# Kernel tuning notes

Measured on AMD Instinct MI355X. Metric: run time of the kernel, lower is better.

The kernel has to match this reference:

```python
import jax, jax.numpy as jnp
import numpy as np

B, S, D, H = 1, 3072, 2048, 16
HD = D // H          # head_dim = 128
C = HD // 2          # rotary complex pairs = 64
EPS = 1e-6
WINDOW = 3           # frames of sliding-window attention on each side
L_TOKENS = 256       # tokens per frame (forward arg L)
NUM_FRAMES = S // L_TOKENS


def setup_inputs() -> dict:
    key = jax.random.key(0)
    ks = jax.random.split(key, 5)
    scale = 1.0 / np.sqrt(D)
    x = jax.random.normal(ks[0], (B, S, D), jnp.float32)
    wq = jax.random.normal(ks[1], (D, D), jnp.float32) * scale
    wk = jax.random.normal(ks[2], (D, D), jnp.float32) * scale
    wv = jax.random.normal(ks[3], (D, D), jnp.float32) * scale
    wo = jax.random.normal(ks[4], (D, D), jnp.float32) * scale
    bq = jnp.zeros((D,), jnp.float32)
    bk = jnp.zeros((D,), jnp.float32)
    bv = jnp.zeros((D,), jnp.float32)
    bo = jnp.zeros((D,), jnp.float32)
    gq = jnp.ones((D,), jnp.float32)
    gk = jnp.ones((D,), jnp.float32)
    # rotary freqs as cos/sin of angle t * theta_c (source uses a complex [S,1,C] tensor)
    t = jnp.arange(S, dtype=jnp.float32)
    inv_freq = 1.0 / (10000.0 ** (jnp.arange(C, dtype=jnp.float32) / C))
    ang = t[:, None] * inv_freq[None, :]        # [S, C]
    cos = jnp.cos(ang)[:, None, :]              # [S, 1, C]
    sin = jnp.sin(ang)[:, None, :]              # [S, 1, C]
    return {"x": x, "wq": wq, "bq": bq, "wk": wk, "bk": bk, "wv": wv,
            "bv": bv, "wo": wo, "bo": bo, "gq": gq, "gk": gk,
            "cos": cos, "sin": sin, "f": NUM_FRAMES, "L": L_TOKENS}


def _rms_norm(h, g, eps=EPS):
    # tensor_parallel_rms_norm with tp_size=1: fp32 variance, rsqrt, scale by weight
    hf = h.astype(jnp.float32)
    var = jnp.mean(hf * hf, axis=-1, keepdims=True)
    return (hf * jax.lax.rsqrt(var + eps) * g).astype(h.dtype)


def _rope(h, cos, sin):
    # complex rotation on interleaved (real, imag) pairs per head (rope_apply_for3d)
    b, s, d = h.shape
    hd = 2 * cos.shape[-1]
    n = d // hd
    hr = h.reshape(b, s, n, hd)
    xr, xi = hr[..., 0::2], hr[..., 1::2]       # [b,s,n,C]
    c, sn = cos[None], sin[None]                # [1,s,1,C] broadcast over heads
    yr = xr * c - xi * sn
    yi = xr * sn + xi * c
    y = jnp.stack([yr, yi], axis=-1).reshape(b, s, n, hd)
    return y.reshape(b, s, d)


def reference(x, wq, bq, wk, bk, wv, bv, wo, bo, gq, gk, cos, sin, f, L):
    q = _rope(_rms_norm(x @ wq.T + bq, gq), cos, sin)
    k = _rope(_rms_norm(x @ wk.T + bk, gk), cos, sin)
    v = x @ wv.T + bv
    b, s, d = q.shape
    hd = 2 * cos.shape[-1]
    n = d // hd
    qh = q.reshape(b, s, n, hd)
    kh = k.reshape(b, s, n, hd)
    vh = v.reshape(b, s, n, hd)
    scale = 1.0 / np.sqrt(hd)
    scores = jnp.einsum('bqnd,bknd->bnqk', qh, kh) * scale
    win = L * WINDOW
    idx = jnp.arange(s)
    delta = idx[None, :] - idx[:, None]
    mask = (delta <= win) & (delta >= -win)
    scores = jnp.where(mask[None, None], scores, -jnp.inf)
    probs = jax.nn.softmax(scores, axis=-1)
    out = jnp.einsum('bnqk,bknd->bqnd', probs, vh).reshape(b, s, d)
    return out @ wo.T + bo
```

## Files before the change

### kernel.cpp

```cpp
#include <hip/hip_runtime.h>
#include <stdint.h>

typedef unsigned short u16;
typedef __attribute__((ext_vector_type(8))) short short8;
typedef __attribute__((ext_vector_type(4))) float f32x4;

#define S_LEN 3072
#define D_DIM 2048
#define WIN 768
#define INV_SQRT_HD 0.08838834764831845f
#define M_SHIFT 12.0f

__device__ __forceinline__ u16 f2bf(float x) {
  union { float f; uint32_t u; } v; v.f = x;
  uint32_t r = v.u + 0x7FFFu + ((v.u >> 16) & 1u);
  return (u16)(r >> 16);
}
__device__ __forceinline__ float bf2f(u16 x) {
  union { uint32_t u; float f; } v; v.u = ((uint32_t)x) << 16;
  return v.f;
}

__device__ __forceinline__ void load_lds16(const void* g, void* l) {
  __builtin_amdgcn_global_load_lds(
      (const __attribute__((address_space(1))) void*)g,
      (__attribute__((address_space(3))) void*)l, 16, 0, 0);
}

#define MFMA16(a, b, c) __builtin_amdgcn_mfma_f32_16x16x32_bf16((a), (b), (c), 0, 0, 0)

__global__ __launch_bounds__(256) void k_cvt_all(const float* __restrict__ x,
                                                 const float* __restrict__ w0, const float* __restrict__ w1,
                                                 const float* __restrict__ w2, const float* __restrict__ w3,
                                                 const float* __restrict__ bq, const float* __restrict__ bk,
                                                 const float* __restrict__ bv,
                                                 u16* __restrict__ xo,
                                                 u16* __restrict__ o0, u16* __restrict__ o1,
                                                 u16* __restrict__ o2, u16* __restrict__ o3,
                                                 float* __restrict__ bias_all,
                                                 int n4x, int n4w) {
  int i = blockIdx.x * 256 + threadIdx.x;
  if (i < n4x + 4 * n4w) {
    const float* in;
    u16* out;
    int off;
    if (i < n4x) {
      in = x; out = xo; off = i;
    } else {
      int j = i - n4x;
      int seg = j / n4w;
      off = j - seg * n4w;
      in = seg == 0 ? w0 : seg == 1 ? w1 : seg == 2 ? w2 : w3;
      out = seg == 0 ? o0 : seg == 1 ? o1 : seg == 2 ? o2 : o3;
    }
    float4 v = ((const float4*)in)[off];
    ushort4 o;
    o.x = f2bf(v.x); o.y = f2bf(v.y); o.z = f2bf(v.z); o.w = f2bf(v.w);
    ((ushort4*)out)[off] = o;
  } else {
    int j = i - n4x - 4 * n4w;
    int seg = j >> 9, off = j & 511;
    const float* in = seg == 0 ? bq : seg == 1 ? bk : bv;
    ((float4*)bias_all)[j] = ((const float4*)in)[off];
  }
}

__global__ __launch_bounds__(256, 3) void k_gemm_qkv(const u16* __restrict__ A,
                                                     const u16* __restrict__ Ball,
                                                     const float* __restrict__ bias_all,
                                                     u16* __restrict__ QKV) {
  __shared__ u16 lA[128 * 32];
  __shared__ u16 lB[192 * 32];
  const int id = blockIdx.x;
  const int xcd = id & 7, local = id >> 3;
  const int m_idx = xcd * 3 + local / 32;
  const int n_idx = local % 32;
  const int m0 = m_idx * 128;
  const int n0g = n_idx * 192;
  const int t = threadIdx.x;
  const int lane = t & 63, w = t >> 6, lo = lane & 15, g = lane >> 4;
  const int wr = w >> 1, wc = w & 1;

  const int srow = t >> 2;
  const int sch = (t & 3) ^ ((srow ^ (srow >> 3)) & 3);
  const u16* ga = A + (size_t)(m0 + srow) * D_DIM + sch * 8;
  const u16* gb = Ball + (size_t)(n0g + srow) * D_DIM + sch * 8;

  const f32x4 zero4 = {0.f, 0.f, 0.f, 0.f};
  f32x4 acc[4][6];
#pragma unroll
  for (int m = 0; m < 4; ++m)
#pragma unroll
    for (int n = 0; n < 6; ++n) acc[m][n] = zero4;

  for (int k0 = 0; k0 < D_DIM; k0 += 32) {
    load_lds16(ga + k0, &lA[t * 8]);
    load_lds16(ga + (size_t)64 * D_DIM + k0, &lA[2048 + t * 8]);
    load_lds16(gb + k0, &lB[t * 8]);
    load_lds16(gb + (size_t)64 * D_DIM + k0, &lB[2048 + t * 8]);
    load_lds16(gb + (size_t)128 * D_DIM + k0, &lB[4096 + t * 8]);
    __syncthreads();
    short8 af[4], bfr[6];
#pragma unroll
    for (int m = 0; m < 4; ++m) {
      const int R = wr * 64 + m * 16 + lo;
      af[m] = *(const short8*)&lA[R * 32 + ((g ^ ((R ^ (R >> 3)) & 3)) << 3)];
    }
#pragma unroll
    for (int n = 0; n < 6; ++n) {
      const int R = wc * 96 + n * 16 + lo;
      bfr[n] = *(const short8*)&lB[R * 32 + ((g ^ ((R ^ (R >> 3)) & 3)) << 3)];
    }
#pragma unroll
    for (int m = 0; m < 4; ++m)
#pragma unroll
      for (int n = 0; n < 6; ++n) acc[m][n] = MFMA16(af[m], bfr[n], acc[m][n]);
    __syncthreads();
  }

#pragma unroll
  for (int m = 0; m < 4; ++m) {
    const int row = m0 + wr * 64 + m * 16 + 4 * g;
#pragma unroll
    for (int n = 0; n < 6; ++n) {
      const int col_g = n0g + wc * 96 + n * 16 + lo;
      const int seg_c = col_g >> 11, c = col_g & 2047;
      u16* D = QKV + (size_t)seg_c * S_LEN * D_DIM;
      const float bb = bias_all[col_g];
#pragma unroll
      for (int r = 0; r < 4; ++r)
        D[(size_t)(row + r) * D_DIM + c] = f2bf(acc[m][n][r] + bb);
    }
  }
}

__device__ __forceinline__ void gemm_body(const u16* __restrict__ A, const u16* __restrict__ B,
                                          int m0, int n0, int t, f32x4 (*acc)[4],
                                          u16* lA, u16* lB) {
  const int lane = t & 63, w = t >> 6, lo = lane & 15, g = lane >> 4;
  const int wr = w >> 1, wc = w & 1;
  const int srow = t >> 2;
  const int sch = (t & 3) ^ ((srow ^ (srow >> 3)) & 3);
  const u16* ga = A + (size_t)(m0 + srow) * D_DIM + sch * 8;
  const u16* gb = B + (size_t)(n0 + srow) * D_DIM + sch * 8;
  for (int k0 = 0; k0 < D_DIM; k0 += 32) {
    load_lds16(ga + k0, &lA[t * 8]);
    load_lds16(ga + (size_t)64 * D_DIM + k0, &lA[2048 + t * 8]);
    load_lds16(gb + k0, &lB[t * 8]);
    load_lds16(gb + (size_t)64 * D_DIM + k0, &lB[2048 + t * 8]);
    __syncthreads();
    short8 af[4], bfr[4];
#pragma unroll
    for (int m = 0; m < 4; ++m) {
      const int R = wr * 64 + m * 16 + lo;
      af[m] = *(const short8*)&lA[R * 32 + ((g ^ ((R ^ (R >> 3)) & 3)) << 3)];
    }
#pragma unroll
    for (int n = 0; n < 4; ++n) {
      const int R = wc * 64 + n * 16 + lo;
      bfr[n] = *(const short8*)&lB[R * 32 + ((g ^ ((R ^ (R >> 3)) & 3)) << 3)];
    }
#pragma unroll
    for (int m = 0; m < 4; ++m)
#pragma unroll
      for (int n = 0; n < 4; ++n) acc[m][n] = MFMA16(af[m], bfr[n], acc[m][n]);
    __syncthreads();
  }
}

__global__ __launch_bounds__(256) void k_gemm_wo(const u16* __restrict__ A,
                                                 const u16* __restrict__ B,
                                                 const float* __restrict__ bias,
                                                 float* __restrict__ C) {
  __shared__ u16 lA[128 * 32];
  __shared__ u16 lB[128 * 32];
  const int id = blockIdx.x;
  const int xcd = id & 7, local = id >> 3;
  const int m_idx = xcd * 3 + local / 16;
  const int n_idx = local % 16;
  const int m0 = m_idx * 128, n0 = n_idx * 128;
  const int t = threadIdx.x;
  const int lane = t & 63, w = t >> 6, lo = lane & 15, g = lane >> 4;
  const int wr = w >> 1, wc = w & 1;
  const f32x4 zero4 = {0.f, 0.f, 0.f, 0.f};
  f32x4 acc[4][4];
#pragma unroll
  for (int m = 0; m < 4; ++m)
#pragma unroll
    for (int n = 0; n < 4; ++n) acc[m][n] = zero4;
  gemm_body(A, B, m0, n0, t, acc, lA, lB);
#pragma unroll
  for (int m = 0; m < 4; ++m) {
    const int row = m0 + wr * 64 + m * 16 + 4 * g;
#pragma unroll
    for (int n = 0; n < 4; ++n) {
      const int col = n0 + wc * 64 + n * 16 + lo;
      const float bb = bias[col];
#pragma unroll
      for (int r = 0; r < 4; ++r)
        C[(size_t)(row + r) * 2048 + col] = acc[m][n][r] + bb;
    }
  }
}

__global__ __launch_bounds__(256) void k_rms_rope2(const u16* __restrict__ Q0, const u16* __restrict__ K0,
                                                   const float* __restrict__ gq, const float* __restrict__ gk,
                                                   const float* __restrict__ cosT, const float* __restrict__ sinT,
                                                   u16* __restrict__ qo, u16* __restrict__ ko) {
  const int s = blockIdx.x, t = threadIdx.x;
  const u16* H = blockIdx.y ? K0 : Q0;
  const float* gain = blockIdx.y ? gk : gq;
  u16* out = blockIdx.y ? ko : qo;
  const short8 hv = *(const short8*)(H + (size_t)s * D_DIM + t * 8);
  float h[8];
#pragma unroll
  for (int j = 0; j < 8; ++j) h[j] = bf2f((u16)hv[j]);
  float ss = 0.f;
#pragma unroll
  for (int j = 0; j < 8; ++j) ss += h[j] * h[j];
#pragma unroll
  for (int off = 32; off > 0; off >>= 1) ss += __shfl_xor(ss, off);
  __shared__ float red[4];
  if ((t & 63) == 0) red[t >> 6] = ss;
  __syncthreads();
  ss = red[0] + red[1] + red[2] + red[3];
  const float rs = rsqrtf(ss * (1.f / D_DIM) + 1e-6f);
  const float4 g0 = *(const float4*)(gain + t * 8);
  const float4 g1 = *(const float4*)(gain + t * 8 + 4);
  float y[8];
  y[0] = h[0] * rs * g0.x; y[1] = h[1] * rs * g0.y;
  y[2] = h[2] * rs * g0.z; y[3] = h[3] * rs * g0.w;
  y[4] = h[4] * rs * g1.x; y[5] = h[5] * rs * g1.y;
  y[6] = h[6] * rs * g1.z; y[7] = h[7] * rs * g1.w;
  const int cbase = ((t * 8) & 127) >> 1;
  short8 o8;
#pragma unroll
  for (int i = 0; i < 4; ++i) {
    const float cs = cosT[s * 64 + cbase + i];
    const float sn = sinT[s * 64 + cbase + i];
    const float yr = y[2 * i] * cs - y[2 * i + 1] * sn;
    const float yi = y[2 * i] * sn + y[2 * i + 1] * cs;
    o8[2 * i] = (short)f2bf(yr);
    o8[2 * i + 1] = (short)f2bf(yi);
  }
  *(short8*)(out + (size_t)s * D_DIM + t * 8) = o8;
}

__global__ __launch_bounds__(256) void k_transpose(const u16* __restrict__ in,
                                                   u16* __restrict__ out) {
  __shared__ u16 tile[64][72];
  const int s0 = blockIdx.x * 64, d0 = blockIdx.y * 64;
  const int t = threadIdx.x;
  const int r = t >> 3, c8 = (t & 7) * 8;
#pragma unroll
  for (int p = 0; p < 2; ++p) {
    short8 v = *(const short8*)&in[(size_t)(s0 + r + p * 32) * D_DIM + d0 + c8];
#pragma unroll
    for (int j = 0; j < 8; ++j) tile[r + p * 32][c8 + j] = (u16)v[j];
  }
  __syncthreads();
#pragma unroll
  for (int p = 0; p < 2; ++p) {
    const int dr = r + p * 32;
    short8 o;
#pragma unroll
    for (int j = 0; j < 8; ++j) o[j] = (short)tile[c8 + j][dr];
    *(short8*)&out[(size_t)(d0 + dr) * S_LEN + s0 + c8] = o;
  }
}

__global__ __launch_bounds__(256, 3) void k_attn5(const u16* __restrict__ Q,
                                                  const u16* __restrict__ Kmat,
                                                  const u16* __restrict__ Vt,
                                                  u16* __restrict__ Oa,
                                                  u16* __restrict__ Ob,
                                                  float* __restrict__ lbuf) {
  const int qt = blockIdx.x, h = blockIdx.y, z = blockIdx.z;
  const int t = threadIdx.x, w = t >> 6, lane = t & 63, lo = lane & 15, g = lane >> 4;
  const int q0 = qt * 128;
  const int wrow = q0 + w * 32;
  const size_t hoff = (size_t)h * 128;

  __shared__ u16 lK[2][32 * 128];
  __shared__ u16 lV[2][128 * 32];
  __shared__ u16 ldsp[4][32][40];

  short8 qf[2][4];
#pragma unroll
  for (int m = 0; m < 2; ++m) {
    const u16* qp = Q + (size_t)(wrow + m * 16 + lo) * D_DIM + hoff + g * 8;
#pragma unroll
    for (int c = 0; c < 4; ++c) qf[m][c] = *(const short8*)(qp + c * 32);
  }

  const f32x4 zero4 = {0.f, 0.f, 0.f, 0.f};
  f32x4 oacc[2][8];
#pragma unroll
  for (int m = 0; m < 2; ++m)
#pragma unroll
    for (int ct = 0; ct < 8; ++ct) oacc[m][ct] = zero4;
  float lrun[2][4] = {{0.f, 0.f, 0.f, 0.f}, {0.f, 0.f, 0.f, 0.f}};

  int jlo = q0 - WIN; if (jlo < 0) jlo = 0;
  int jhi = q0 + 127 + WIN + 1; if (jhi > S_LEN) jhi = S_LEN;
  const int NT = (jhi - jlo) >> 5;
  const int it0 = z * (NT >> 1), it1 = it0 + (NT >> 1);

  const int krow = t >> 4,          kch  = (t & 15) ^ (krow & 7);
  const int krow1 = (t + 256) >> 4, kch1 = (t & 15) ^ (krow1 & 7);
  const int vrow = t >> 2,          vch  = (t & 3) ^ ((vrow >> 1) & 3);
  const int vrow1 = (t + 256) >> 2, vch1 = (t & 3) ^ ((vrow1 >> 1) & 3);

#define STAGE5(buf, jj)                                                                              \
  do {                                                                                               \
    load_lds16(Kmat + (size_t)((jj) + krow) * D_DIM + hoff + (kch << 3), &lK[buf][t * 8]);           \
    load_lds16(Kmat + (size_t)((jj) + krow1) * D_DIM + hoff + (kch1 << 3), &lK[buf][(t + 256) * 8]); \
    load_lds16(Vt + (size_t)(hoff + vrow) * S_LEN + (jj) + (vch << 3), &lV[buf][t * 8]);             \
    load_lds16(Vt + (size_t)(hoff + vrow1) * S_LEN + (jj) + (vch1 << 3), &lV[buf][(t + 256) * 8]);   \
  } while (0)

  STAGE5(0, jlo + (it0 << 5));
  __syncthreads();
  int cur = 0;
  for (int it = it0; it < it1; ++it) {
    const int j0 = jlo + (it << 5);
    if (it + 1 < it1) STAGE5(cur ^ 1, j0 + 32);

    f32x4 sc[2][2];
    sc[0][0] = zero4; sc[0][1] = zero4; sc[1][0] = zero4; sc[1][1] = zero4;
#pragma unroll
    for (int half = 0; half < 2; ++half) {
#pragma unroll
      for (int c = 0; c < 4; ++c) {
        const short8 kf = *(const short8*)
            &lK[cur][(half * 16 + lo) * 128 + (((g + 4 * c) ^ (lo & 7)) << 3)];
        sc[0][half] = MFMA16(qf[0][c], kf, sc[0][half]);
        sc[1][half] = MFMA16(qf[1][c], kf, sc[1][half]);
      }
    }

    const int dq = j0 - q0;
    const bool interior = (dq >= -640) && (dq <= 736);
#pragma unroll
    for (int m = 0; m < 2; ++m) {
#pragma unroll
      for (int r = 0; r < 4; ++r) {
        float a0 = fmaf(sc[m][0][r], INV_SQRT_HD, -M_SHIFT);
        float a1 = fmaf(sc[m][1][r], INV_SQRT_HD, -M_SHIFT);
        if (!interior) {
          const int dk = j0 + lo - (wrow + m * 16 + 4 * g + r);
          if (dk < -WIN || dk > WIN) a0 = -3e38f;
          if (dk + 16 < -WIN || dk + 16 > WIN) a1 = -3e38f;
        }
        const float p0 = __expf(a0);
        const float p1 = __expf(a1);
        lrun[m][r] += p0 + p1;
        ldsp[w][m * 16 + 4 * g + r][lo] = f2bf(p0);
        ldsp[w][m * 16 + 4 * g + r][16 + lo] = f2bf(p1);
      }
    }

    const short8 pf0 = *(const short8*)&ldsp[w][lo][g * 8];
    const short8 pf1 = *(const short8*)&ldsp[w][16 + lo][g * 8];
#pragma unroll
    for (int ct = 0; ct < 8; ++ct) {
      const short8 vf = *(const short8*)
          &lV[cur][(ct * 16 + lo) * 32 + ((g ^ ((lo >> 1) & 3)) << 3)];
      oacc[0][ct] = MFMA16(pf0, vf, oacc[0][ct]);
      oacc[1][ct] = MFMA16(pf1, vf, oacc[1][ct]);
    }
    __syncthreads();
    cur ^= 1;
  }
#undef STAGE5

#pragma unroll
  for (int off = 8; off > 0; off >>= 1)
#pragma unroll
    for (int m = 0; m < 2; ++m)
#pragma unroll
      for (int r = 0; r < 4; ++r) lrun[m][r] += __shfl_xor(lrun[m][r], off);

  u16* Op = z ? Ob : Oa;
#pragma unroll
  for (int m = 0; m < 2; ++m)
#pragma unroll
    for (int r = 0; r < 4; ++r) {
      const int row = wrow + m * 16 + 4 * g + r;
#pragma unroll
      for (int ct = 0; ct < 8; ++ct)
        Op[(size_t)row * D_DIM + hoff + ct * 16 + lo] = f2bf(oacc[m][ct][r]);
      if (lo == 0) lbuf[(size_t)z * S_LEN * 16 + (size_t)row * 16 + h] = lrun[m][r];
    }
}

__global__ __launch_bounds__(256) void k_combine(const u16* __restrict__ Oa,
                                                 const u16* __restrict__ Ob,
                                                 const float* __restrict__ lbuf,
                                                 u16* __restrict__ out) {
  const int i = blockIdx.x * 256 + threadIdx.x;
  const int s = i >> 8, d8 = (i & 255) * 8, h = d8 >> 7;
  const float la = lbuf[(size_t)s * 16 + h];
  const float lb = lbuf[(size_t)S_LEN * 16 + (size_t)s * 16 + h];
  const float inv = 1.f / (la + lb);
  const size_t base = (size_t)s * D_DIM + d8;
  const short8 a = *(const short8*)(Oa + base);
  const short8 b = *(const short8*)(Ob + base);
  short8 o;
#pragma unroll
  for (int j = 0; j < 8; ++j)
    o[j] = (short)f2bf((bf2f((u16)a[j]) + bf2f((u16)b[j])) * inv);
  *(short8*)(out + base) = o;
}

extern "C" void kernel_launch(void* const* d_in, const int* in_sizes, int n_in,
                              void* d_out, int out_size, void* d_ws, size_t ws_size,
                              hipStream_t stream) {
  const float* x    = (const float*)d_in[0];
  const float* wq   = (const float*)d_in[1];
  const float* bq   = (const float*)d_in[2];
  const float* wk   = (const float*)d_in[3];
  const float* bk   = (const float*)d_in[4];
  const float* wv   = (const float*)d_in[5];
  const float* bv   = (const float*)d_in[6];
  const float* wo   = (const float*)d_in[7];
  const float* bo   = (const float*)d_in[8];
  const float* gq   = (const float*)d_in[9];
  const float* gk   = (const float*)d_in[10];
  const float* cosT = (const float*)d_in[11];
  const float* sinT = (const float*)d_in[12];

  char* ws = (char*)d_ws;
  const size_t WB = (size_t)D_DIM * D_DIM * 2;
  const size_t XB = (size_t)S_LEN * D_DIM * 2;
  u16*   wq_bf = (u16*)(ws);
  u16*   wk_bf = (u16*)(ws + WB);
  u16*   wv_bf = (u16*)(ws + 2 * WB);
  u16*   wo_bf = (u16*)(ws + 3 * WB);
  u16*   x_bf  = (u16*)(ws + 4 * WB);
  u16*   Q0b   = (u16*)(ws + 4 * WB + XB);
  u16*   K0b   = (u16*)(ws + 4 * WB + 2 * XB);
  u16*   V0b   = (u16*)(ws + 4 * WB + 3 * XB);
  float* lbuf  = (float*)(ws + 4 * WB + 4 * XB);
  float* bias_all = (float*)(ws + 4 * WB + 4 * XB + 512 * 1024);
  u16* q_bf = x_bf;
  u16* k_bf = wq_bf;
  u16* vT   = Q0b;
  u16* Ob   = K0b;
  u16* Oa   = (u16*)d_out;
  u16* attn = V0b;

  const int nw4 = (D_DIM * D_DIM) / 4;
  const int nx4 = (S_LEN * D_DIM) / 4;
  const int ncvt = nx4 + 4 * nw4 + 6144 / 4;
  k_cvt_all<<<ncvt / 256, 256, 0, stream>>>(
      x, wq, wk, wv, wo, bq, bk, bv, x_bf, wq_bf, wk_bf, wv_bf, wo_bf, bias_all, nx4, nw4);

  k_gemm_qkv<<<768, 256, 0, stream>>>(x_bf, wq_bf, bias_all, Q0b);

  k_rms_rope2<<<dim3(S_LEN, 2), 256, 0, stream>>>(Q0b, K0b, gq, gk, cosT, sinT, q_bf, k_bf);
  k_transpose<<<dim3(S_LEN / 64, D_DIM / 64), 256, 0, stream>>>(V0b, vT);

  k_attn5<<<dim3(S_LEN / 128, 16, 2), 256, 0, stream>>>(q_bf, k_bf, vT, Oa, Ob, lbuf);
  k_combine<<<(S_LEN * D_DIM / 8) / 256, 256, 0, stream>>>(Oa, Ob, lbuf, attn);

  k_gemm_wo<<<384, 256, 0, stream>>>(attn, wo_bf, bo, (float*)d_out);
}
```

Measured before the change: 228.8 us.

## Merge RMS-rope and V transpose into one launch; remap attention blocks per XCD

The RMS-norm plus rotary kernel and the V transpose kernel now run as one launch, with a block-index split deciding which job each block does. This removes a kernel launch and lets the two jobs share the GPU at the same time. The attention grid is flattened to 1D and remapped so each of the 8 XCDs (chosen by the low bits of the block id) handles two whole heads, which should improve L2 reuse of K/V. vT moves to a separate workspace slot because Q0b is read in the same kernel that writes vT. The risk is that the two job types in the merged kernel balance poorly across the GPU.

```diff
diff --git a/kernel.cpp b/kernel.cpp
--- a/kernel.cpp
+++ b/kernel.cpp
@@ -203,69 +203,71 @@
   }
 }
 
-__global__ __launch_bounds__(256) void k_rms_rope2(const u16* __restrict__ Q0, const u16* __restrict__ K0,
-                                                   const float* __restrict__ gq, const float* __restrict__ gk,
-                                                   const float* __restrict__ cosT, const float* __restrict__ sinT,
-                                                   u16* __restrict__ qo, u16* __restrict__ ko) {
-  const int s = blockIdx.x, t = threadIdx.x;
-  const u16* H = blockIdx.y ? K0 : Q0;
-  const float* gain = blockIdx.y ? gk : gq;
-  u16* out = blockIdx.y ? ko : qo;
-  const short8 hv = *(const short8*)(H + (size_t)s * D_DIM + t * 8);
-  float h[8];
-#pragma unroll
-  for (int j = 0; j < 8; ++j) h[j] = bf2f((u16)hv[j]);
-  float ss = 0.f;
-#pragma unroll
-  for (int j = 0; j < 8; ++j) ss += h[j] * h[j];
-#pragma unroll
-  for (int off = 32; off > 0; off >>= 1) ss += __shfl_xor(ss, off);
-  __shared__ float red[4];
-  if ((t & 63) == 0) red[t >> 6] = ss;
-  __syncthreads();
-  ss = red[0] + red[1] + red[2] + red[3];
-  const float rs = rsqrtf(ss * (1.f / D_DIM) + 1e-6f);
-  const float4 g0 = *(const float4*)(gain + t * 8);
-  const float4 g1 = *(const float4*)(gain + t * 8 + 4);
-  float y[8];
-  y[0] = h[0] * rs * g0.x; y[1] = h[1] * rs * g0.y;
-  y[2] = h[2] * rs * g0.z; y[3] = h[3] * rs * g0.w;
-  y[4] = h[4] * rs * g1.x; y[5] = h[5] * rs * g1.y;
-  y[6] = h[6] * rs * g1.z; y[7] = h[7] * rs * g1.w;
-  const int cbase = ((t * 8) & 127) >> 1;
-  short8 o8;
-#pragma unroll
-  for (int i = 0; i < 4; ++i) {
-    const float cs = cosT[s * 64 + cbase + i];
-    const float sn = sinT[s * 64 + cbase + i];
-    const float yr = y[2 * i] * cs - y[2 * i + 1] * sn;
-    const float yi = y[2 * i] * sn + y[2 * i + 1] * cs;
-    o8[2 * i] = (short)f2bf(yr);
-    o8[2 * i + 1] = (short)f2bf(yi);
-  }
-  *(short8*)(out + (size_t)s * D_DIM + t * 8) = o8;
-}
-
-__global__ __launch_bounds__(256) void k_transpose(const u16* __restrict__ in,
-                                                   u16* __restrict__ out) {
-  __shared__ u16 tile[64][72];
-  const int s0 = blockIdx.x * 64, d0 = blockIdx.y * 64;
-  const int t = threadIdx.x;
-  const int r = t >> 3, c8 = (t & 7) * 8;
-#pragma unroll
-  for (int p = 0; p < 2; ++p) {
-    short8 v = *(const short8*)&in[(size_t)(s0 + r + p * 32) * D_DIM + d0 + c8];
-#pragma unroll
-    for (int j = 0; j < 8; ++j) tile[r + p * 32][c8 + j] = (u16)v[j];
-  }
-  __syncthreads();
-#pragma unroll
-  for (int p = 0; p < 2; ++p) {
-    const int dr = r + p * 32;
-    short8 o;
-#pragma unroll
-    for (int j = 0; j < 8; ++j) o[j] = (short)tile[c8 + j][dr];
-    *(short8*)&out[(size_t)(d0 + dr) * S_LEN + s0 + c8] = o;
+__global__ __launch_bounds__(256) void k_aux(const u16* __restrict__ Q0, const u16* __restrict__ K0,
+                                             const u16* __restrict__ V0,
+                                             const float* __restrict__ gq, const float* __restrict__ gk,
+                                             const float* __restrict__ cosT, const float* __restrict__ sinT,
+                                             u16* __restrict__ qo, u16* __restrict__ ko,
+                                             u16* __restrict__ vT) {
+  const int bid = blockIdx.x, t = threadIdx.x;
+  if (bid < 2 * S_LEN) {
+    const int s = bid >> 1, which = bid & 1;
+    const u16* H = which ? K0 : Q0;
+    const float* gain = which ? gk : gq;
+    u16* out = which ? ko : qo;
+    const short8 hv = *(const short8*)(H + (size_t)s * D_DIM + t * 8);
+    float h[8];
+#pragma unroll
+    for (int j = 0; j < 8; ++j) h[j] = bf2f((u16)hv[j]);
+    float ss = 0.f;
+#pragma unroll
+    for (int j = 0; j < 8; ++j) ss += h[j] * h[j];
+#pragma unroll
+    for (int off = 32; off > 0; off >>= 1) ss += __shfl_xor(ss, off);
+    __shared__ float red[4];
+    if ((t & 63) == 0) red[t >> 6] = ss;
+    __syncthreads();
+    ss = red[0] + red[1] + red[2] + red[3];
+    const float rs = rsqrtf(ss * (1.f / D_DIM) + 1e-6f);
+    const float4 g0 = *(const float4*)(gain + t * 8);
+    const float4 g1 = *(const float4*)(gain + t * 8 + 4);
+    float y[8];
+    y[0] = h[0] * rs * g0.x; y[1] = h[1] * rs * g0.y;
+    y[2] = h[2] * rs * g0.z; y[3] = h[3] * rs * g0.w;
+    y[4] = h[4] * rs * g1.x; y[5] = h[5] * rs * g1.y;
+    y[6] = h[6] * rs * g1.z; y[7] = h[7] * rs * g1.w;
+    const int cbase = ((t * 8) & 127) >> 1;
+    short8 o8;
+#pragma unroll
+    for (int i = 0; i < 4; ++i) {
+      const float cs = cosT[s * 64 + cbase + i];
+      const float sn = sinT[s * 64 + cbase + i];
+      const float yr = y[2 * i] * cs - y[2 * i + 1] * sn;
+      const float yi = y[2 * i] * sn + y[2 * i + 1] * cs;
+      o8[2 * i] = (short)f2bf(yr);
+      o8[2 * i + 1] = (short)f2bf(yi);
+    }
+    *(short8*)(out + (size_t)s * D_DIM + t * 8) = o8;
+  } else {
+    __shared__ u16 tile[64][72];
+    const int idx = bid - 2 * S_LEN;
+    const int s0 = (idx % 48) * 64, d0 = (idx / 48) * 64;
+    const int r = t >> 3, c8 = (t & 7) * 8;
+#pragma unroll
+    for (int p = 0; p < 2; ++p) {
+      short8 v = *(const short8*)&V0[(size_t)(s0 + r + p * 32) * D_DIM + d0 + c8];
+#pragma unroll
+      for (int j = 0; j < 8; ++j) tile[r + p * 32][c8 + j] = (u16)v[j];
+    }
+    __syncthreads();
+#pragma unroll
+    for (int p = 0; p < 2; ++p) {
+      const int dr = r + p * 32;
+      short8 o;
+#pragma unroll
+      for (int j = 0; j < 8; ++j) o[j] = (short)tile[c8 + j][dr];
+      *(short8*)&vT[(size_t)(d0 + dr) * S_LEN + s0 + c8] = o;
+    }
   }
 }
 
@@ -275,7 +277,11 @@
                                                   u16* __restrict__ Oa,
                                                   u16* __restrict__ Ob,
                                                   float* __restrict__ lbuf) {
-  const int qt = blockIdx.x, h = blockIdx.y, z = blockIdx.z;
+  const int id = blockIdx.x;
+  const int xcd = id & 7, local = id >> 3;
+  const int h = xcd * 2 + (local / 48);
+  const int rr_ = local % 48;
+  const int qt = rr_ >> 1, z = rr_ & 1;
   const int t = threadIdx.x, w = t >> 6, lane = t & 63, lo = lane & 15, g = lane >> 4;
   const int q0 = qt * 128;
   const int wrow = q0 + w * 32;
@@ -445,7 +451,7 @@
   float* bias_all = (float*)(ws + 4 * WB + 4 * XB + 512 * 1024);
   u16* q_bf = x_bf;
   u16* k_bf = wq_bf;
-  u16* vT   = Q0b;
+  u16* vT   = (u16*)(ws + XB);
   u16* Ob   = K0b;
   u16* Oa   = (u16*)d_out;
   u16* attn = V0b;
@@ -458,10 +464,9 @@
 
   k_gemm_qkv<<<768, 256, 0, stream>>>(x_bf, wq_bf, bias_all, Q0b);
 
-  k_rms_rope2<<<dim3(S_LEN, 2), 256, 0, stream>>>(Q0b, K0b, gq, gk, cosT, sinT, q_bf, k_bf);
-  k_transpose<<<dim3(S_LEN / 64, D_DIM / 64), 256, 0, stream>>>(V0b, vT);
-
-  k_attn5<<<dim3(S_LEN / 128, 16, 2), 256, 0, stream>>>(q_bf, k_bf, vT, Oa, Ob, lbuf);
+  k_aux<<<2 * S_LEN + 1536, 256, 0, stream>>>(Q0b, K0b, V0b, gq, gk, cosT, sinT, q_bf, k_bf, vT);
+
+  k_attn5<<<768, 256, 0, stream>>>(q_bf, k_bf, vT, Oa, Ob, lbuf);
   k_combine<<<(S_LEN * D_DIM / 8) / 256, 256, 0, stream>>>(Oa, Ob, lbuf, attn);
 
   k_gemm_wo<<<384, 256, 0, stream>>>(attn, wo_bf, bo, (float*)d_out);
```

After: 221.6 us. 3.1% less time.
